# Kernel tuning notes

Measured on AMD Instinct MI355X. Metric: run time of the kernel, lower is better.

The kernel has to match this reference:

```python
import jax, jax.numpy as jnp
import numpy as np
from jax import lax

D_MODEL = 1024
D_FF = 4096
K = 5
PAD = K // 2


def setup_inputs() -> dict:
    key = jax.random.key(0)
    ks = jax.random.split(key, 12)
    s_in = 1.0 / np.sqrt(D_MODEL)
    s_ff = 1.0 / np.sqrt(D_FF)
    s_k = 1.0 / np.sqrt(K)  # depthwise conv fan_in = 1*K
    return {
        "x": jax.random.normal(ks[0], (4, 2048, D_MODEL), dtype=jnp.float32),
        "Wg": jax.random.uniform(ks[1], (D_MODEL, D_FF), jnp.float32, -s_in, s_in),
        "bg": jax.random.uniform(ks[2], (D_FF,), jnp.float32, -s_in, s_in),
        "Wu": jax.random.uniform(ks[3], (D_MODEL, D_FF), jnp.float32, -s_in, s_in),
        "bu": jax.random.uniform(ks[4], (D_FF,), jnp.float32, -s_in, s_in),
        "convg_w": jax.random.uniform(ks[5], (D_FF, 1, K), jnp.float32, -s_k, s_k),
        "convg_b": jax.random.uniform(ks[6], (D_FF,), jnp.float32, -s_k, s_k),
        "convu_w": jax.random.uniform(ks[7], (D_FF, 1, K), jnp.float32, -s_k, s_k),
        "convu_b": jax.random.uniform(ks[8], (D_FF,), jnp.float32, -s_k, s_k),
        "Wd": jax.random.uniform(ks[9], (D_FF, D_MODEL), jnp.float32, -s_ff, s_ff),
        "bd": jax.random.uniform(ks[10], (D_MODEL,), jnp.float32, -s_ff, s_ff),
    }


def _dwconv(h, w, b):
    # h: [B, L, C] -> depthwise conv along L with 'same' padding -> [B, L, C]
    y = lax.conv_general_dilated(
        h.transpose(0, 2, 1),  # [B, C, L]
        w,                      # [C, 1, K]
        window_strides=(1,),
        padding=[(PAD, PAD)],
        feature_group_count=h.shape[-1],
    )
    return (y + b[None, :, None]).transpose(0, 2, 1)


def reference(x, Wg, bg, Wu, bu, convg_w, convg_b, convu_w, convu_b, Wd, bd):
    gate = _dwconv(jnp.einsum("bld,df->blf", x, Wg) + bg, convg_w, convg_b)
    up = _dwconv(jnp.einsum("bld,df->blf", x, Wu) + bu, convu_w, convu_b)
    h = jax.nn.silu(gate) * up
    return jnp.einsum("blf,fd->bld", h, Wd) + bd
```

## Files before the change

kernel.cpp:

```cpp
#include <hip/hip_runtime.h>
#include <hip/hip_bf16.h>
#include <cstdint>

#define BATCH  4
#define SEQ    2048
#define DMODEL 1024
#define DFF    4096
#define MTOT   (BATCH * SEQ)
#define KCONV  5
#define PADC   2

using bf16raw = unsigned short;
typedef __attribute__((ext_vector_type(8))) short bf16x8;
typedef __attribute__((ext_vector_type(4))) float f32x4;

__device__ __forceinline__ float bf2f(bf16raw u) {
    return __uint_as_float(((uint32_t)u) << 16);
}
__device__ __forceinline__ bf16raw f2bf(float f) {
    uint32_t u = __float_as_uint(f);
    u = (u + 0x7fffu + ((u >> 16) & 1u)) >> 16;
    return (bf16raw)u;
}


__global__ __launch_bounds__(256)
void cvt_bf16_kernel(const float* __restrict__ in, bf16raw* __restrict__ out, int n4)
{
    const int i = blockIdx.x * 256 + threadIdx.x;
    if (i >= n4) return;
    const float4 v = reinterpret_cast<const float4*>(in)[i];
    ushort4 o;
    o.x = f2bf(v.x); o.y = f2bf(v.y); o.z = f2bf(v.z); o.w = f2bf(v.w);
    reinterpret_cast<ushort4*>(out)[i] = o;
}

__global__ __launch_bounds__(256)
void transpose_cvt_kernel(const float* __restrict__ in, bf16raw* __restrict__ out,
                          int R, int C)
{
    __shared__ float tile[32][33];
    const int r0 = blockIdx.y * 32, c0 = blockIdx.x * 32;
    const int tx = threadIdx.x & 31, ty = threadIdx.x >> 5;
#pragma unroll
    for (int i = 0; i < 4; ++i)
        tile[ty + i * 8][tx] = in[(size_t)(r0 + ty + i * 8) * C + c0 + tx];
    __syncthreads();
#pragma unroll
    for (int i = 0; i < 4; ++i)
        out[(size_t)(c0 + ty + i * 8) * R + r0 + tx] = f2bf(tile[tx][ty + i * 8]);
}

__global__ __launch_bounds__(256)
void convw_reorder_kernel(const float* __restrict__ wg, const float* __restrict__ wu,
                          float* __restrict__ wgT, float* __restrict__ wuT)
{
    const int i = blockIdx.x * 256 + threadIdx.x;
    if (i >= KCONV * DFF) return;
    const int j = i / DFF, f = i - j * DFF;
    wgT[i] = wg[f * KCONV + j];
    wuT[i] = wu[f * KCONV + j];
}


__device__ __forceinline__ void gll16(const bf16raw* g, const char* lds)
{
    __builtin_amdgcn_global_load_lds(
        (const __attribute__((address_space(1))) void*)g,
        (__attribute__((address_space(3))) void*)lds, 16, 0, 0);
}

template<typename CT, bool BIAS, int SPLITK, bool COLMAJOR>
__global__ __launch_bounds__(512, 2)
void gemmp_kernel(const bf16raw* __restrict__ A, const bf16raw* __restrict__ BT,
                  const float* __restrict__ bias0, const float* __restrict__ bias1,
                  CT* __restrict__ C, int M, int N, int K, int nbm, int nbn)
{
    __shared__ __align__(16) char smem[131072];

    const int tid  = threadIdx.x;
    const int lane = tid & 63;
    const int wave = __builtin_amdgcn_readfirstlane(tid >> 6);
    const int wr = wave >> 2;
    const int wc = wave & 3;

    const int bid = blockIdx.x;
    int sk = 0, rem = bid;
    if constexpr (SPLITK > 1) { sk = rem / (nbm * nbn); rem = rem - sk * (nbm * nbn); }
    int bx, by;
    if constexpr (COLMAJOR) { bx = rem / nbm; by = rem - bx * nbm; }
    else                    { by = rem / nbn; bx = rem - by * nbn; }
    const int bm = by * 256;
    const int bn = bx * 256;

    const int klen = K / SPLITK;
    const int kbeg = sk * klen;
    const int NT   = klen / 32;
    CT* Cp = C + (size_t)sk * M * N;

    const int srow  = tid >> 2;
    const int sphys = tid & 3;

    auto stage = [&](int t) {
#pragma unroll
        for (int half = 0; half < 2; ++half) {
            const int row = half * 128 + srow;
            gll16(A + (size_t)(bm + row) * K + kbeg + t * 32
                    + ((sphys ^ ((row >> 1) & 3)) << 3),
                  smem + (size_t)(t & 3) * 32768 + row * 64 + sphys * 16);
        }
#pragma unroll
        for (int half = 0; half < 2; ++half) {
            const int row = half * 128 + srow;
            gll16(BT + (size_t)(bn + row) * K + kbeg + t * 32
                    + ((sphys ^ ((row >> 1) & 3)) << 3),
                  smem + (size_t)(t & 3) * 32768 + 16384 + row * 64 + sphys * 16);
        }
    };

    const int g4   = lane >> 4;
    const int r15  = lane & 15;
    const int koff = ((g4 ^ ((r15 >> 1) & 3)) << 4);

    auto ldA = [&](int buf, int mf) -> bf16x8 {
        return *(const bf16x8*)(smem + (size_t)buf * 32768
                                + (wr * 128 + mf * 16 + r15) * 64 + koff);
    };
    auto ldB = [&](int buf, int nf) -> bf16x8 {
        return *(const bf16x8*)(smem + (size_t)buf * 32768 + 16384
                                + (wc * 64 + nf * 16 + r15) * 64 + koff);
    };

    f32x4 acc[8][4];
#pragma unroll
    for (int i = 0; i < 8; ++i)
#pragma unroll
        for (int j = 0; j < 4; ++j) acc[i][j] = (f32x4){0.f, 0.f, 0.f, 0.f};

    bf16x8 A0[2], A1[2], Bb0[4], Bb1[4];

#define MFMA_SET(M0, ASET, BSET)                                               \
    __builtin_amdgcn_s_setprio(1);                                             \
    _Pragma("unroll")                                                          \
    for (int i_ = 0; i_ < 2; ++i_)                                             \
        _Pragma("unroll")                                                      \
        for (int nf_ = 0; nf_ < 4; ++nf_)                                      \
            acc[(M0) + i_][nf_] = __builtin_amdgcn_mfma_f32_16x16x32_bf16(     \
                ASET[i_], BSET[nf_], acc[(M0) + i_][nf_], 0, 0, 0);            \
    __builtin_amdgcn_s_setprio(0);

#define TILE_BODY(T, BC, BN)                                                   \
    {                                                                          \
        const int t_   = (T);                                                  \
        const int buf_ = t_ & 3;                                               \
                                 \
        A1[0] = ldA(buf_, 2); A1[1] = ldA(buf_, 3);                            \
        MFMA_SET(0, A0, BC)                                                    \
                                 \
        A0[0] = ldA(buf_, 4); A0[1] = ldA(buf_, 5);                            \
        MFMA_SET(2, A1, BC)                                                    \
                                 \
        A1[0] = ldA(buf_, 6); A1[1] = ldA(buf_, 7);                            \
        MFMA_SET(4, A0, BC)                                                    \
                     \
        if (t_ + 2 < NT) asm volatile("s_waitcnt vmcnt(4)" ::: "memory");      \
        else             asm volatile("s_waitcnt vmcnt(0)" ::: "memory");      \
        __builtin_amdgcn_s_barrier();                                          \
        asm volatile("" ::: "memory");                                         \
        if (t_ + 3 < NT) stage(t_ + 3);                                        \
                       \
        if (t_ + 1 < NT) {                                                     \
            const int nb_ = (t_ + 1) & 3;                                      \
            BN[0] = ldB(nb_, 0); BN[1] = ldB(nb_, 1);                          \
            BN[2] = ldB(nb_, 2); BN[3] = ldB(nb_, 3);                          \
            A0[0] = ldA(nb_, 0); A0[1] = ldA(nb_, 1);                          \
        }                                                                      \
        MFMA_SET(6, A1, BC)                                                    \
        asm volatile("" ::: "memory");                                         \
    }

    stage(0);
    if (NT > 1) stage(1);
    if (NT > 2) stage(2);
    if (NT > 2)      asm volatile("s_waitcnt vmcnt(8)" ::: "memory");
    else if (NT > 1) asm volatile("s_waitcnt vmcnt(4)" ::: "memory");
    else             asm volatile("s_waitcnt vmcnt(0)" ::: "memory");
    __builtin_amdgcn_s_barrier();
    asm volatile("" ::: "memory");
    Bb0[0] = ldB(0, 0); Bb0[1] = ldB(0, 1); Bb0[2] = ldB(0, 2); Bb0[3] = ldB(0, 3);
    A0[0]  = ldA(0, 0); A0[1]  = ldA(0, 1);

    for (int tt = 0; tt < NT; tt += 2) {
        TILE_BODY(tt, Bb0, Bb1)
        if (tt + 1 < NT) TILE_BODY(tt + 1, Bb1, Bb0)
    }
#undef TILE_BODY
#undef MFMA_SET

    const int er = g4 << 2;
#pragma unroll
    for (int nf = 0; nf < 4; ++nf) {
        const int nn = bn + wc * 64 + nf * 16 + r15;
        float bv = 0.f;
        if constexpr (BIAS) bv = (nn < DFF) ? bias0[nn] : bias1[nn - DFF];
#pragma unroll
        for (int mf = 0; mf < 8; ++mf) {
            const int mrow = bm + wr * 128 + mf * 16 + er;
#pragma unroll
            for (int j = 0; j < 4; ++j) {
                const float v = acc[mf][nf][j] + bv;
                if constexpr (sizeof(CT) == 2)
                    Cp[(size_t)(mrow + j) * N + nn] = f2bf(v);
                else
                    Cp[(size_t)(mrow + j) * N + nn] = v;
            }
        }
    }
}

template<int NS>
__global__ __launch_bounds__(256)
void reduce_bias_kernel(const float* __restrict__ part, const float* __restrict__ bd,
                        float* __restrict__ out)
{
    const int i = blockIdx.x * 256 + threadIdx.x;
    const int d = (i & (DMODEL / 4 - 1)) * 4;
    const float4 bb = *reinterpret_cast<const float4*>(bd + d);
    float4 o; o.x = bb.x; o.y = bb.y; o.z = bb.z; o.w = bb.w;
#pragma unroll
    for (int s = 0; s < NS; ++s) {
        const float4 a = reinterpret_cast<const float4*>(part + (size_t)s * MTOT * DMODEL)[i];
        o.x += a.x; o.y += a.y; o.z += a.z; o.w += a.w;
    }
    reinterpret_cast<float4*>(out)[i] = o;
}

__global__ __launch_bounds__(256)
void conv_silu_mul_bf16_kernel(const bf16raw* __restrict__ gp, const bf16raw* __restrict__ up,
                               const float* __restrict__ wgT, const float* __restrict__ cbg,
                               const float* __restrict__ wuT, const float* __restrict__ cbu,
                               bf16raw* __restrict__ h, int S)
{
    const int idx = blockIdx.x * 256 + threadIdx.x;
    const int f   = (idx & (DFF / 8 - 1)) << 3;
    const int row = idx >> 9;
    const int l   = row & (SEQ - 1);
    const int rb  = row - l;

    float g[8], u[8];
    {
        const float4 a0 = *reinterpret_cast<const float4*>(cbg + f);
        const float4 a1 = *reinterpret_cast<const float4*>(cbg + f + 4);
        const float4 b0 = *reinterpret_cast<const float4*>(cbu + f);
        const float4 b1 = *reinterpret_cast<const float4*>(cbu + f + 4);
        g[0]=a0.x; g[1]=a0.y; g[2]=a0.z; g[3]=a0.w; g[4]=a1.x; g[5]=a1.y; g[6]=a1.z; g[7]=a1.w;
        u[0]=b0.x; u[1]=b0.y; u[2]=b0.z; u[3]=b0.w; u[4]=b1.x; u[5]=b1.y; u[6]=b1.z; u[7]=b1.w;
    }

#pragma unroll
    for (int j = 0; j < KCONV; ++j) {
        const int ls = l + j - PADC;
        if (ls < 0 || ls >= SEQ) continue;
        const size_t off = (size_t)(rb + ls) * S + f;
        const bf16x8 gv = *reinterpret_cast<const bf16x8*>(gp + off);
        const bf16x8 uv = *reinterpret_cast<const bf16x8*>(up + off);
        const float4 wa0 = *reinterpret_cast<const float4*>(wgT + j * DFF + f);
        const float4 wa1 = *reinterpret_cast<const float4*>(wgT + j * DFF + f + 4);
        const float4 wb0 = *reinterpret_cast<const float4*>(wuT + j * DFF + f);
        const float4 wb1 = *reinterpret_cast<const float4*>(wuT + j * DFF + f + 4);
        const float wg8[8] = {wa0.x, wa0.y, wa0.z, wa0.w, wa1.x, wa1.y, wa1.z, wa1.w};
        const float wu8[8] = {wb0.x, wb0.y, wb0.z, wb0.w, wb1.x, wb1.y, wb1.z, wb1.w};
#pragma unroll
        for (int c = 0; c < 8; ++c) {
            g[c] += bf2f((bf16raw)gv[c]) * wg8[c];
            u[c] += bf2f((bf16raw)uv[c]) * wu8[c];
        }
    }

    bf16x8 hv;
#pragma unroll
    for (int c = 0; c < 8; ++c) {
        const float s = g[c] / (1.f + __expf(-g[c]));
        hv[c] = (short)f2bf(s * u[c]);
    }
    *reinterpret_cast<bf16x8*>(h + (size_t)row * DFF + f) = hv;
}


#define BM 128
#define BN 128
#define BK 8

__device__ __forceinline__ void load4f(const float* p, float v[4]) {
    const float4 t = *reinterpret_cast<const float4*>(p);
    v[0] = t.x; v[1] = t.y; v[2] = t.z; v[3] = t.w;
}

__global__ __launch_bounds__(256)
void sgemm_bias_kernel(const float* __restrict__ A, const float* __restrict__ B,
                       const float* __restrict__ bias, float* __restrict__ C,
                       int N, int K)
{
    __shared__ float As[BK][BM];
    __shared__ float Bs[BK][BN];

    const int tid = threadIdx.x;
    const int bm  = blockIdx.y * BM;
    const int bn  = blockIdx.x * BN;
    const int tx  = tid & 15;
    const int ty  = tid >> 4;

    const int arow = tid >> 1;
    const int acol = (tid & 1) * 4;
    const int brow = tid >> 5;
    const int bcol = (tid & 31) * 4;

    const float* Ap = A + (size_t)(bm + arow) * K + acol;
    const float* Bp = B + (size_t)brow * N + bn + bcol;

    float acc[8][8];
#pragma unroll
    for (int i = 0; i < 8; ++i)
#pragma unroll
        for (int j = 0; j < 8; ++j) acc[i][j] = 0.f;

    for (int k0 = 0; k0 < K; k0 += BK) {
        float av[4];
        load4f(Ap + k0, av);
        const float4 bv = *reinterpret_cast<const float4*>(Bp + (size_t)k0 * N);
        __syncthreads();
#pragma unroll
        for (int i = 0; i < 4; ++i) As[acol + i][arow] = av[i];
        *reinterpret_cast<float4*>(&Bs[brow][bcol]) = bv;
        __syncthreads();
#pragma unroll
        for (int kk = 0; kk < BK; ++kk) {
            const float4 a0 = *reinterpret_cast<const float4*>(&As[kk][ty * 4]);
            const float4 a1 = *reinterpret_cast<const float4*>(&As[kk][64 + ty * 4]);
            const float4 b0 = *reinterpret_cast<const float4*>(&Bs[kk][tx * 4]);
            const float4 b1 = *reinterpret_cast<const float4*>(&Bs[kk][64 + tx * 4]);
            const float am[8] = {a0.x, a0.y, a0.z, a0.w, a1.x, a1.y, a1.z, a1.w};
            const float bb[8] = {b0.x, b0.y, b0.z, b0.w, b1.x, b1.y, b1.z, b1.w};
#pragma unroll
            for (int mi = 0; mi < 8; ++mi)
#pragma unroll
                for (int nj = 0; nj < 8; ++nj)
                    acc[mi][nj] += am[mi] * bb[nj];
        }
    }
#pragma unroll
    for (int mi = 0; mi < 8; ++mi) {
        const int m = bm + ((mi < 4) ? (ty * 4 + mi) : (64 + ty * 4 + (mi - 4)));
#pragma unroll
        for (int g = 0; g < 2; ++g) {
            const int n = bn + g * 64 + tx * 4;
            float4 o;
            o.x = acc[mi][g * 4 + 0] + bias[n + 0];
            o.y = acc[mi][g * 4 + 1] + bias[n + 1];
            o.z = acc[mi][g * 4 + 2] + bias[n + 2];
            o.w = acc[mi][g * 4 + 3] + bias[n + 3];
            *reinterpret_cast<float4*>(&C[(size_t)m * N + n]) = o;
        }
    }
}

__global__ __launch_bounds__(256)
void conv_silu_mul_f32_kernel(const float* __restrict__ gp, const float* __restrict__ up,
                              const float* __restrict__ wg, const float* __restrict__ cbg,
                              const float* __restrict__ wu, const float* __restrict__ cbu,
                              float* __restrict__ hout)
{
    const int idx = blockIdx.x * 256 + threadIdx.x;
    const int f   = (idx & (DFF / 4 - 1)) * 4;
    const int l   = idx >> 10;

    float g[4], u[4];
    load4f(cbg + f, g);
    load4f(cbu + f, u);
#pragma unroll
    for (int j = 0; j < KCONV; ++j) {
        const int ls = l + j - PADC;
        if (ls < 0 || ls >= SEQ) continue;
        const size_t off = (size_t)ls * DFF + f;
        float gv[4], uv[4];
        load4f(gp + off, gv);
        load4f(up + off, uv);
#pragma unroll
        for (int c = 0; c < 4; ++c) {
            g[c] += gv[c] * wg[(f + c) * KCONV + j];
            u[c] += uv[c] * wu[(f + c) * KCONV + j];
        }
    }
    float h[4];
#pragma unroll
    for (int c = 0; c < 4; ++c) {
        const float s = g[c] / (1.f + __expf(-g[c]));
        h[c] = s * u[c];
    }
    float4 o; o.x = h[0]; o.y = h[1]; o.z = h[2]; o.w = h[3];
    *reinterpret_cast<float4*>(&hout[(size_t)l * DFF + f]) = o;
}


extern "C" void kernel_launch(void* const* d_in, const int* in_sizes, int n_in,
                              void* d_out, int out_size, void* d_ws, size_t ws_size,
                              hipStream_t stream)
{
    const float* x   = (const float*)d_in[0];
    const float* Wg  = (const float*)d_in[1];
    const float* bg  = (const float*)d_in[2];
    const float* Wu  = (const float*)d_in[3];
    const float* bu  = (const float*)d_in[4];
    const float* cgw = (const float*)d_in[5];
    const float* cgb = (const float*)d_in[6];
    const float* cuw = (const float*)d_in[7];
    const float* cub = (const float*)d_in[8];
    const float* Wd  = (const float*)d_in[9];
    const float* bd  = (const float*)d_in[10];
    float* out = (float*)d_out;

    const dim3 blk(256);
    auto align256 = [](size_t v) { return (v + 255) & ~(size_t)255; };

    const size_t SZ_XB  = (size_t)MTOT * DMODEL * 2;
    const size_t SZ_WGU = (size_t)2 * DFF * DMODEL * 2;
    const size_t SZ_WD  = (size_t)DMODEL * DFF * 2;
    const size_t SZ_CW  = (size_t)KCONV * DFF * 4;
    const size_t SZ_H   = (size_t)MTOT * DFF * 2;
    const size_t SZ_UP  = (size_t)MTOT * 2 * DFF * 2;

    size_t cur = 0;
    const size_t oXB  = cur; cur = align256(cur + SZ_XB);
    const size_t oWGU = cur; cur = align256(cur + SZ_WGU);
    const size_t oWD  = cur; cur = align256(cur + SZ_WD);
    const size_t oCWg = cur; cur = align256(cur + SZ_CW);
    const size_t oCWu = cur; cur = align256(cur + SZ_CW);
    const size_t oH   = cur; cur = align256(cur + SZ_H);
    const size_t oUP  = cur; cur = align256(cur + SZ_UP);
    const size_t need = cur;

    if (ws_size >= need) {
        bf16raw* xb   = (bf16raw*)((char*)d_ws + oXB);
        bf16raw* Wgu  = (bf16raw*)((char*)d_ws + oWGU);
        bf16raw* WdT  = (bf16raw*)((char*)d_ws + oWD);
        float*   cwg  = (float*)((char*)d_ws + oCWg);
        float*   cwu  = (float*)((char*)d_ws + oCWu);
        bf16raw* h    = (bf16raw*)((char*)d_ws + oH);
        bf16raw* Cup  = (bf16raw*)((char*)d_ws + oUP);
        float*   part = (float*)((char*)d_ws + oUP);

        cvt_bf16_kernel<<<(MTOT * DMODEL / 4 + 255) / 256, blk, 0, stream>>>(x, xb, MTOT * DMODEL / 4);
        transpose_cvt_kernel<<<dim3(DFF / 32, DMODEL / 32), blk, 0, stream>>>(Wg, Wgu, DMODEL, DFF);
        transpose_cvt_kernel<<<dim3(DFF / 32, DMODEL / 32), blk, 0, stream>>>(Wu, Wgu + (size_t)DFF * DMODEL, DMODEL, DFF);
        transpose_cvt_kernel<<<dim3(DMODEL / 32, DFF / 32), blk, 0, stream>>>(Wd, WdT, DFF, DMODEL);
        convw_reorder_kernel<<<(KCONV * DFF + 255) / 256, blk, 0, stream>>>(cgw, cuw, cwg, cwu);

        {
            const int nbm = MTOT / 256, nbn = (2 * DFF) / 256;
            gemmp_kernel<bf16raw, true, 1, false><<<nbm * nbn, dim3(512), 0, stream>>>(
                xb, Wgu, bg, bu, Cup, MTOT, 2 * DFF, DMODEL, nbm, nbn);
        }

        conv_silu_mul_bf16_kernel<<<MTOT * (DFF / 8) / 256, blk, 0, stream>>>(
            Cup, Cup + DFF, cwg, cgb, cwu, cub, h, 2 * DFF);

        {
            const int nbm = MTOT / 256, nbn = DMODEL / 256;
            gemmp_kernel<float, false, 2, false><<<nbm * nbn * 2, dim3(512), 0, stream>>>(
                h, WdT, nullptr, nullptr, part, MTOT, DMODEL, DFF, nbm, nbn);
        }
        reduce_bias_kernel<2><<<MTOT * DMODEL / 4 / 256, blk, 0, stream>>>(part, bd, out);
        return;
    }

    const size_t CE  = (size_t)SEQ * DFF;
    const size_t P32 = CE * sizeof(float);
    if (ws_size < 3 * P32) return;

    float* gpre = (float*)d_ws;
    float* upre = gpre + CE;
    float* hbuf = upre + CE;
    dim3 gu(DFF / BN, SEQ / BM);
    dim3 gdc(DMODEL / BN, SEQ / BM);
    const int nconv = SEQ * (DFF / 4) / 256;
    for (int b = 0; b < BATCH; ++b) {
        const float* xbp = x + (size_t)b * SEQ * DMODEL;
        float* outb = out + (size_t)b * SEQ * DMODEL;
        sgemm_bias_kernel<<<gu, blk, 0, stream>>>(xbp, Wg, bg, gpre, DFF, DMODEL);
        sgemm_bias_kernel<<<gu, blk, 0, stream>>>(xbp, Wu, bu, upre, DFF, DMODEL);
        conv_silu_mul_f32_kernel<<<nconv, blk, 0, stream>>>(gpre, upre, cgw, cgb, cuw, cub, hbuf);
        sgemm_bias_kernel<<<gdc, blk, 0, stream>>>(hbuf, Wd, bd, outb, DMODEL, DFF);
    }
}
```

Before: 387.7 us.

## Replace split-K down-projection GEMM and reduce with single 128x128 tile kernel

Swaps the down-projection from a 256x256-tile split-K GEMM plus a separate bias-reduce kernel for a new 128x128-tile GEMM with 256 threads that writes the final output with bias added directly. This drops the fp32 partial buffer write/read and one kernel launch, and gives 512 blocks instead of 256 for parallelism. The new kernel is single-buffered: it loads a tile, waits on vmcnt(0) and barriers, then computes, so there is no load/compute overlap and reuse per block is lower than before.

```diff
diff --git a/kernel.cpp b/kernel.cpp
--- a/kernel.cpp
+++ b/kernel.cpp
@@ -62,13 +62,13 @@
     wuT[i] = wu[f * KCONV + j];
 }
 
-
 __device__ __forceinline__ void gll16(const bf16raw* g, const char* lds)
 {
     __builtin_amdgcn_global_load_lds(
         (const __attribute__((address_space(1))) void*)g,
         (__attribute__((address_space(3))) void*)lds, 16, 0, 0);
 }
+
 
 template<typename CT, bool BIAS, int SPLITK, bool COLMAJOR>
 __global__ __launch_bounds__(512, 2)
@@ -153,22 +153,17 @@
     {                                                                          \
         const int t_   = (T);                                                  \
         const int buf_ = t_ & 3;                                               \
-                                 \
         A1[0] = ldA(buf_, 2); A1[1] = ldA(buf_, 3);                            \
         MFMA_SET(0, A0, BC)                                                    \
-                                 \
         A0[0] = ldA(buf_, 4); A0[1] = ldA(buf_, 5);                            \
         MFMA_SET(2, A1, BC)                                                    \
-                                 \
         A1[0] = ldA(buf_, 6); A1[1] = ldA(buf_, 7);                            \
         MFMA_SET(4, A0, BC)                                                    \
-                     \
         if (t_ + 2 < NT) asm volatile("s_waitcnt vmcnt(4)" ::: "memory");      \
         else             asm volatile("s_waitcnt vmcnt(0)" ::: "memory");      \
         __builtin_amdgcn_s_barrier();                                          \
         asm volatile("" ::: "memory");                                         \
         if (t_ + 3 < NT) stage(t_ + 3);                                        \
-                       \
         if (t_ + 1 < NT) {                                                     \
             const int nb_ = (t_ + 1) & 3;                                      \
             BN[0] = ldB(nb_, 0); BN[1] = ldB(nb_, 1);                          \
@@ -218,21 +213,100 @@
     }
 }
 
-template<int NS>
-__global__ __launch_bounds__(256)
-void reduce_bias_kernel(const float* __restrict__ part, const float* __restrict__ bd,
-                        float* __restrict__ out)
-{
-    const int i = blockIdx.x * 256 + threadIdx.x;
-    const int d = (i & (DMODEL / 4 - 1)) * 4;
-    const float4 bb = *reinterpret_cast<const float4*>(bd + d);
-    float4 o; o.x = bb.x; o.y = bb.y; o.z = bb.z; o.w = bb.w;
-#pragma unroll
-    for (int s = 0; s < NS; ++s) {
-        const float4 a = reinterpret_cast<const float4*>(part + (size_t)s * MTOT * DMODEL)[i];
-        o.x += a.x; o.y += a.y; o.z += a.z; o.w += a.w;
-    }
-    reinterpret_cast<float4*>(out)[i] = o;
+
+__global__ __launch_bounds__(256, 3)
+void gemm97_kernel(const bf16raw* __restrict__ A, const bf16raw* __restrict__ BT,
+                   const float* __restrict__ bias, float* __restrict__ out,
+                   int N, int K, int nbn)
+{
+    __shared__ __align__(16) char smem[32768];
+
+    const int tid  = threadIdx.x;
+    const int lane = tid & 63;
+    const int wave = __builtin_amdgcn_readfirstlane(tid >> 6);
+    const int wr = wave >> 1;
+    const int wc = wave & 1;
+
+    const int bid = blockIdx.x;
+    const int bx = bid % nbn;
+    const int by = bid / nbn;
+    const int bm = by * 128;
+    const int bn = bx * 128;
+
+    const int NT = K / 64;
+
+    const int srow32 = tid >> 3;
+    const int chunkp = tid & 7;
+
+    auto stage = [&](int t) {
+#pragma unroll
+        for (int r = 0; r < 4; ++r) {
+            const int row = r * 32 + srow32;
+            gll16(A + (size_t)(bm + row) * K + t * 64 + ((chunkp ^ (row & 7)) << 3),
+                  smem + r * 4096 + tid * 16);
+        }
+#pragma unroll
+        for (int r = 0; r < 4; ++r) {
+            const int row = r * 32 + srow32;
+            gll16(BT + (size_t)(bn + row) * K + t * 64 + ((chunkp ^ (row & 7)) << 3),
+                  smem + 16384 + r * 4096 + tid * 16);
+        }
+    };
+
+    const int g4  = lane >> 4;
+    const int r15 = lane & 15;
+    const int key = r15 & 7;
+
+    f32x4 acc[4][4];
+#pragma unroll
+    for (int i = 0; i < 4; ++i)
+#pragma unroll
+        for (int j = 0; j < 4; ++j) acc[i][j] = (f32x4){0.f, 0.f, 0.f, 0.f};
+
+    for (int t = 0; t < NT; ++t) {
+        stage(t);
+        asm volatile("s_waitcnt vmcnt(0)" ::: "memory");
+        __builtin_amdgcn_s_barrier();
+#pragma unroll
+        for (int kk = 0; kk < 2; ++kk) {
+            const int cl = kk * 4 + g4;
+            bf16x8 b[4], a[4];
+#pragma unroll
+            for (int nf = 0; nf < 4; ++nf) {
+                const int row = wc * 64 + nf * 16 + r15;
+                b[nf] = *(const bf16x8*)(smem + 16384 + row * 128
+                                         + ((cl ^ (row & 7)) << 4));
+            }
+#pragma unroll
+            for (int mf = 0; mf < 4; ++mf) {
+                const int row = wr * 64 + mf * 16 + r15;
+                a[mf] = *(const bf16x8*)(smem + row * 128 + ((cl ^ (row & 7)) << 4));
+            }
+            __builtin_amdgcn_s_setprio(1);
+#pragma unroll
+            for (int mf = 0; mf < 4; ++mf)
+#pragma unroll
+                for (int nf = 0; nf < 4; ++nf)
+                    acc[mf][nf] = __builtin_amdgcn_mfma_f32_16x16x32_bf16(
+                        a[mf], b[nf], acc[mf][nf], 0, 0, 0);
+            __builtin_amdgcn_s_setprio(0);
+        }
+        __builtin_amdgcn_s_barrier();
+    }
+
+    const int er = g4 << 2;
+#pragma unroll
+    for (int nf = 0; nf < 4; ++nf) {
+        const int nn = bn + wc * 64 + nf * 16 + r15;
+        const float bv = bias[nn];
+#pragma unroll
+        for (int mf = 0; mf < 4; ++mf) {
+            const int mrow = bm + wr * 64 + mf * 16 + er;
+#pragma unroll
+            for (int j = 0; j < 4; ++j)
+                out[(size_t)(mrow + j) * N + nn] = acc[mf][nf][j] + bv;
+        }
+    }
 }
 
 __global__ __launch_bounds__(256)
@@ -447,7 +521,6 @@
         float*   cwu  = (float*)((char*)d_ws + oCWu);
         bf16raw* h    = (bf16raw*)((char*)d_ws + oH);
         bf16raw* Cup  = (bf16raw*)((char*)d_ws + oUP);
-        float*   part = (float*)((char*)d_ws + oUP);
 
         cvt_bf16_kernel<<<(MTOT * DMODEL / 4 + 255) / 256, blk, 0, stream>>>(x, xb, MTOT * DMODEL / 4);
         transpose_cvt_kernel<<<dim3(DFF / 32, DMODEL / 32), blk, 0, stream>>>(Wg, Wgu, DMODEL, DFF);
@@ -465,11 +538,10 @@
             Cup, Cup + DFF, cwg, cgb, cwu, cub, h, 2 * DFF);
 
         {
-            const int nbm = MTOT / 256, nbn = DMODEL / 256;
-            gemmp_kernel<float, false, 2, false><<<nbm * nbn * 2, dim3(512), 0, stream>>>(
-                h, WdT, nullptr, nullptr, part, MTOT, DMODEL, DFF, nbm, nbn);
-        }
-        reduce_bias_kernel<2><<<MTOT * DMODEL / 4 / 256, blk, 0, stream>>>(part, bd, out);
+            const int nbn = DMODEL / 128;
+            const int nbm = MTOT / 128;
+            gemm97_kernel<<<nbm * nbn, blk, 0, stream>>>(h, WdT, bd, out, DMODEL, DFF, nbn);
+        }
         return;
     }
 
```

After: 388.7 us. Within noise of the previous version (+0.3%).
